# Kernel tuning notes

Measured on AMD Instinct MI355X. Metric: run time of the kernel, lower is better.

Reference implementation:

```python
import jax, jax.numpy as jnp
import numpy as np

B, N, C, K, S = 2, 20000, 64, 16, 4  # batch, points, channels, neighbors, share_planes
CS = C // S
EPS = 1e-5


def _gather(x, idx):
    # x: [B, C, N], idx: [B, N, K] -> [B, C, N, K]
    return jax.vmap(lambda xb, ib: xb[:, ib])(x, idx)


def _bn(x, g, b, m, v):
    # inference-mode BatchNorm2d over channel axis 1; x: [B, C, N, K]
    scale = (g / jnp.sqrt(v + EPS))[None, :, None, None]
    return (x - m[None, :, None, None]) * scale + b[None, :, None, None]


def setup_inputs() -> dict:
    key = jax.random.key(0)
    ks = jax.random.split(key, 32)
    d = {}
    d["coord"] = jax.random.normal(ks[0], (B, N, 3), jnp.float32)
    d["q"] = jax.random.normal(ks[1], (B, C, N), jnp.float32)
    d["k"] = jax.random.normal(ks[2], (B, C, N), jnp.float32)
    d["neighbor_indices"] = jax.random.randint(ks[3], (B, N, K), 0, N, jnp.int32)
    sc = 1.0 / np.sqrt(C)
    d["wq"] = jax.random.normal(ks[4], (C, C), jnp.float32) * sc
    d["bq"] = jnp.zeros((C,), jnp.float32)
    d["wk"] = jax.random.normal(ks[5], (C, C), jnp.float32) * sc
    d["bk"] = jnp.zeros((C,), jnp.float32)
    d["wv"] = jax.random.normal(ks[6], (C, C), jnp.float32) * sc
    d["bv"] = jnp.zeros((C,), jnp.float32)
    # linear_p: Conv2d(3,3,1) -> BN(3) -> ReLU -> Conv2d(3,C,1)
    d["p1_w"] = jax.random.normal(ks[7], (3, 3), jnp.float32) * 0.5
    d["p1_b"] = jnp.zeros((3,), jnp.float32)
    d["p_bn_g"] = jnp.ones((3,), jnp.float32)
    d["p_bn_b"] = jnp.zeros((3,), jnp.float32)
    d["p_bn_m"] = jax.random.normal(ks[8], (3,), jnp.float32) * 0.1
    d["p_bn_v"] = jax.random.uniform(ks[9], (3,), jnp.float32) + 0.5
    d["p2_w"] = jax.random.normal(ks[10], (C, 3), jnp.float32) * 0.5
    d["p2_b"] = jnp.zeros((C,), jnp.float32)
    # linear_w: BN(C) -> ReLU -> Conv2d(C, C//S, 1) -> BN(C//S) -> ReLU -> Conv2d(C//S, C//S, 1)
    d["w_bn1_g"] = jnp.ones((C,), jnp.float32)
    d["w_bn1_b"] = jnp.zeros((C,), jnp.float32)
    d["w_bn1_m"] = jax.random.normal(ks[11], (C,), jnp.float32) * 0.1
    d["w_bn1_v"] = jax.random.uniform(ks[12], (C,), jnp.float32) + 0.5
    d["w1_w"] = jax.random.normal(ks[13], (CS, C), jnp.float32) * sc
    d["w1_b"] = jnp.zeros((CS,), jnp.float32)
    d["w_bn2_g"] = jnp.ones((CS,), jnp.float32)
    d["w_bn2_b"] = jnp.zeros((CS,), jnp.float32)
    d["w_bn2_m"] = jax.random.normal(ks[14], (CS,), jnp.float32) * 0.1
    d["w_bn2_v"] = jax.random.uniform(ks[15], (CS,), jnp.float32) + 0.5
    d["w2_w"] = jax.random.normal(ks[16], (CS, CS), jnp.float32) / np.sqrt(CS)
    d["w2_b"] = jnp.zeros((CS,), jnp.float32)
    return d


def reference(coord, q, k, neighbor_indices, wq, bq, wk, bk, wv, bv,
              p1_w, p1_b, p_bn_g, p_bn_b, p_bn_m, p_bn_v, p2_w, p2_b,
              w_bn1_g, w_bn1_b, w_bn1_m, w_bn1_v, w1_w, w1_b,
              w_bn2_g, w_bn2_b, w_bn2_m, w_bn2_v, w2_w, w2_b):
    # 1x1 Conv1d projections: [B, C, N]
    x_q = jnp.einsum('oc,bcn->bon', wq, q) + bq[None, :, None]
    x_k = jnp.einsum('oc,bcn->bon', wk, k) + bk[None, :, None]
    x_v = jnp.einsum('oc,bcn->bon', wv, q) + bv[None, :, None]
    # KNN gathers -> [B, *, N, K]
    p_r = _gather(jnp.swapaxes(coord, 1, 2), neighbor_indices)  # [B, 3, N, K]
    x_k = _gather(x_k, neighbor_indices)                        # [B, C, N, K]
    x_v = _gather(x_v, neighbor_indices)                        # [B, C, N, K]
    # positional MLP
    p_r = jnp.einsum('oc,bcnk->bonk', p1_w, p_r) + p1_b[None, :, None, None]
    p_r = jax.nn.relu(_bn(p_r, p_bn_g, p_bn_b, p_bn_m, p_bn_v))
    p_r = jnp.einsum('oc,bcnk->bonk', p2_w, p_r) + p2_b[None, :, None, None]  # [B, C, N, K]
    # attention weights MLP
    w = x_k - x_q[:, :, :, None] + p_r                          # [B, C, N, K]
    w = jax.nn.relu(_bn(w, w_bn1_g, w_bn1_b, w_bn1_m, w_bn1_v))
    w = jnp.einsum('oc,bcnk->bonk', w1_w, w) + w1_b[None, :, None, None]      # [B, C/S, N, K]
    w = jax.nn.relu(_bn(w, w_bn2_g, w_bn2_b, w_bn2_m, w_bn2_v))
    w = jnp.einsum('oc,bcnk->bonk', w2_w, w) + w2_b[None, :, None, None]
    w = jax.nn.softmax(w, axis=-1)                              # softmax over K
    # grouped weighted sum
    v = jnp.transpose(x_v + p_r, (0, 2, 3, 1)).reshape(B, N, K, S, CS)  # [B, N, K, S, C/S]
    wp = jnp.transpose(w, (0, 2, 3, 1))                                  # [B, N, K, C/S]
    x = jnp.einsum('bnksg,bnkg->bnsg', v, wp).reshape(B, N, C)
    return jnp.transpose(x, (0, 2, 1))  # [B, C, N]
```

## Files before the change

kernel.cpp:

```cpp
#include <hip/hip_runtime.h>
#include <math.h>

#define B_ 2
#define N_ 20000
#define C_ 64
#define K_ 16
#define CS_ 16
#define EPS_ 1e-5f

typedef float f32x4_t  __attribute__((ext_vector_type(4)));
typedef short bf16x8_t __attribute__((ext_vector_type(8)));
typedef short bf16x4_t __attribute__((ext_vector_type(4)));

__device__ __forceinline__ unsigned int bfbits(float f)
{
    unsigned int b = __builtin_bit_cast(unsigned int, f);
    return (b + 0x7FFFu + ((b >> 16) & 1u)) >> 16;
}
__device__ __forceinline__ float bf_lo(unsigned int w)
{
    return __builtin_bit_cast(float, w << 16);
}
__device__ __forceinline__ float bf_hi(unsigned int w)
{
    return __builtin_bit_cast(float, w & 0xFFFF0000u);
}
__device__ __forceinline__ void wave_fence()
{
    __builtin_amdgcn_wave_barrier();
}
__device__ __forceinline__ unsigned int pk2(const float* p)
{
    return bfbits(p[0]) | (bfbits(p[1]) << 16);
}

__global__ __launch_bounds__(256) void setup_kernel(
    const float* __restrict__ wq, const float* __restrict__ wk,
    const float* __restrict__ wv,
    const float* __restrict__ w1_w, const float* __restrict__ w1_b,
    const float* __restrict__ w2_w, const float* __restrict__ w2_b,
    const float* __restrict__ w_bn2_g, const float* __restrict__ w_bn2_b,
    const float* __restrict__ w_bn2_m, const float* __restrict__ w_bn2_v,
    uint4* __restrict__ wtab, uint4* __restrict__ a1tab,
    uint2* __restrict__ a2tab, float* __restrict__ cz)
{
    const int t = threadIdx.x;
    for (int e = t; e < 1536; e += 256) {
        int m = e >> 9, rem = e & 511;
        int og = rem >> 7, half = (rem >> 6) & 1, l = rem & 63;
        const float* W = (m == 0) ? wq : ((m == 1) ? wk : wv);
        const float* base = W + (size_t)(og * 16 + (l & 15)) * C_ + half * 32 + (l >> 4) * 8;
        uint4 o;
        o.x = pk2(base + 0); o.y = pk2(base + 2);
        o.z = pk2(base + 4); o.w = pk2(base + 6);
        wtab[e] = o;
    }
    if (t < 128) {
        int half = t >> 6, l = t & 63;
        const float* base = w1_w + (size_t)(l & 15) * C_ + half * 32 + (l >> 4) * 8;
        uint4 o;
        o.x = pk2(base + 0); o.y = pk2(base + 2);
        o.z = pk2(base + 4); o.w = pk2(base + 6);
        a1tab[t] = o;
    }
    if (t < 64) {
        const float* base = w2_w + (t & 15) * 16 + (t >> 4) * 4;
        uint2 o;
        o.x = pk2(base + 0); o.y = pk2(base + 2);
        a2tab[t] = o;
    }
    if (t < 16) {
        float s = w_bn2_g[t] * rsqrtf(w_bn2_v[t] + EPS_);
        cz[t]      = s;
        cz[16 + t] = (w1_b[t] - w_bn2_m[t]) * s + w_bn2_b[t];
        cz[32 + t] = w2_b[t];
    }
}

__global__ __launch_bounds__(256) void proj_kernel(
    const float* __restrict__ q, const float* __restrict__ kin,
    const float* __restrict__ coord,
    const float* __restrict__ bq, const float* __restrict__ bk,
    const float* __restrict__ bv,
    const float* __restrict__ p1_w, const float* __restrict__ p1_b,
    const float* __restrict__ p_bn_g, const float* __restrict__ p_bn_b,
    const float* __restrict__ p_bn_m, const float* __restrict__ p_bn_v,
    const float* __restrict__ p2_w, const float* __restrict__ p2_b,
    const float* __restrict__ w_bn1_g, const float* __restrict__ w_bn1_b,
    const float* __restrict__ w_bn1_m, const float* __restrict__ w_bn1_v,
    const uint4* __restrict__ wtab,
    float* __restrict__ xq2, unsigned int* __restrict__ kv_t)
{
    constexpr int PS = 26;
    __shared__ unsigned int qp[32 * PS];
    __shared__ unsigned int kp[32 * PS];

    const int t   = threadIdx.x;
    const int og  = __builtin_amdgcn_readfirstlane(t >> 6);
    const int l   = t & 63;
    const int col = l & 15;
    const int qd  = l >> 4;
    const int pt0 = blockIdx.x * 16;
    const int pt  = pt0 + col;
    const int b   = pt0 / N_;
    const int n   = pt - b * N_;
    const size_t cb = (size_t)b * C_ * N_ + n;

#pragma unroll
    for (int r = 0; r < 2; r++) {
        int cp = (og << 3) + (qd << 1) + r;
        int ci = cp * 2;
        float q0 = q[cb + (size_t)ci * N_];
        float q1 = q[cb + (size_t)(ci + 1) * N_];
        float k0 = kin[cb + (size_t)ci * N_];
        float k1 = kin[cb + (size_t)(ci + 1) * N_];
        qp[cp * PS + col] = bfbits(q0) | (bfbits(q1) << 16);
        kp[cp * PS + col] = bfbits(k0) | (bfbits(k1) << 16);
    }

    union bf8u { bf16x8_t v; uint4 u4; };
    bf8u awq[2], awk[2], awv[2];
#pragma unroll
    for (int half = 0; half < 2; half++) {
        awq[half].u4 = wtab[0 * 512 + og * 128 + half * 64 + l];
        awk[half].u4 = wtab[1 * 512 + og * 128 + half * 64 + l];
        awv[half].u4 = wtab[2 * 512 + og * 128 + half * 64 + l];
    }

    __syncthreads();

    union bf8b { bf16x8_t v; unsigned int u[4]; };
    bf8b bq_[2], bk_[2];
#pragma unroll
    for (int half = 0; half < 2; half++) {
#pragma unroll
        for (int i2 = 0; i2 < 4; i2++) {
            int cp = half * 16 + qd * 4 + i2;
            bq_[half].u[i2] = qp[cp * PS + col];
            bk_[half].u[i2] = kp[cp * PS + col];
        }
    }

    f32x4_t uq = {0.f, 0.f, 0.f, 0.f};
    f32x4_t uv = {0.f, 0.f, 0.f, 0.f};
    f32x4_t uk = {0.f, 0.f, 0.f, 0.f};
    uq = __builtin_amdgcn_mfma_f32_16x16x32_bf16(awq[0].v, bq_[0].v, uq, 0, 0, 0);
    uq = __builtin_amdgcn_mfma_f32_16x16x32_bf16(awq[1].v, bq_[1].v, uq, 0, 0, 0);
    uv = __builtin_amdgcn_mfma_f32_16x16x32_bf16(awv[0].v, bq_[0].v, uv, 0, 0, 0);
    uv = __builtin_amdgcn_mfma_f32_16x16x32_bf16(awv[1].v, bq_[1].v, uv, 0, 0, 0);
    uk = __builtin_amdgcn_mfma_f32_16x16x32_bf16(awk[0].v, bk_[0].v, uk, 0, 0, 0);
    uk = __builtin_amdgcn_mfma_f32_16x16x32_bf16(awk[1].v, bk_[1].v, uk, 0, 0, 0);

    float pbs[3], pbb[3];
#pragma unroll
    for (int j = 0; j < 3; j++) {
        float s = p_bn_g[j] * rsqrtf(p_bn_v[j] + EPS_);
        pbs[j] = s;
        pbb[j] = (p1_b[j] - p_bn_m[j]) * s + p_bn_b[j];
    }
    float cx = coord[pt * 3 + 0], cy = coord[pt * 3 + 1], cz = coord[pt * 3 + 2];
    float h0 = fmaxf(0.f, (p1_w[0]*cx + p1_w[1]*cy + p1_w[2]*cz) * pbs[0] + pbb[0]);
    float h1 = fmaxf(0.f, (p1_w[3]*cx + p1_w[4]*cy + p1_w[5]*cz) * pbs[1] + pbb[1]);
    float h2 = fmaxf(0.f, (p1_w[6]*cx + p1_w[7]*cy + p1_w[8]*cz) * pbs[2] + pbb[2]);

    const int ch0 = og * 16 + qd * 4;
    float pos[4];
#pragma unroll
    for (int rr = 0; rr < 4; rr++) {
        int ch = ch0 + rr;
        pos[rr] = fmaf(p2_w[ch*3+0], h0, fmaf(p2_w[ch*3+1], h1,
                  fmaf(p2_w[ch*3+2], h2, p2_b[ch])));
    }

    const float4 bqv = *reinterpret_cast<const float4*>(bq + ch0);
    const float4 bkv = *reinterpret_cast<const float4*>(bk + ch0);
    const float4 bvv = *reinterpret_cast<const float4*>(bv + ch0);
    const float4 g1  = *reinterpret_cast<const float4*>(w_bn1_g + ch0);
    const float4 b1  = *reinterpret_cast<const float4*>(w_bn1_b + ch0);
    const float4 m1  = *reinterpret_cast<const float4*>(w_bn1_m + ch0);
    const float4 v1  = *reinterpret_cast<const float4*>(w_bn1_v + ch0);

    float4 xqo;
    uint4 kvo;
#pragma unroll
    for (int rr = 0; rr < 4; rr++) {
        float s   = (&g1.x)[rr] * rsqrtf((&v1.x)[rr] + EPS_);
        float b1f = (&b1.x)[rr] - (&m1.x)[rr] * s;
        float xqv = uq[rr] + (&bqv.x)[rr];
        (&xqo.x)[rr] = s * xqv - b1f;
        float kk = s * (uk[rr] + (&bkv.x)[rr] + pos[rr]);
        float vv = uv[rr] + (&bvv.x)[rr] + pos[rr];
        (&kvo.x)[rr] = bfbits(kk) | (bfbits(vv) << 16);
    }
    *reinterpret_cast<float4*>(xq2 + (size_t)pt * C_ + ch0) = xqo;
    *reinterpret_cast<uint4*>(kv_t + (size_t)pt * C_ + ch0) = kvo;
}

#define WROW 72
#define WPN  (K_ * WROW)
#define SS4  20
#define SPN  (K_ * SS4)

__global__ __launch_bounds__(1024, 8) void attn_kernel(
    const int* __restrict__ nbr,
    const float* __restrict__ xq2, const unsigned int* __restrict__ kv_t,
    const uint4* __restrict__ a1tab, const uint2* __restrict__ a2tab,
    const float* __restrict__ cz,
    float* __restrict__ out)
{
    __shared__ unsigned short wlds_all[16 * WPN];
    __shared__ float          sfb_all[16 * SPN];
    __shared__ float          otile[64 * 17];

    const int w  = __builtin_amdgcn_readfirstlane(threadIdx.x >> 6);
    const int l  = threadIdx.x & 63;
    const int al = l & 15;
    const int qd = l >> 4;
    const int cpair = l & 31;
    const int kh    = l >> 5;
    const int c0    = cpair * 2;

    const int pt0 = blockIdx.x * 16;
    const int b   = pt0 / N_;
    const int bB  = b * N_;
    const int bn  = pt0 + w;

    unsigned short* wlds = wlds_all + w * WPN;
    float*          sfb  = sfb_all + w * SPN;

    union bf8u { bf16x8_t v; uint4 u4; };
    union bf4u { bf16x4_t v; uint2 u2; };
    bf8u a1q0, a1q1; bf4u a2q;
    a1q0.u4 = a1tab[l];
    a1q1.u4 = a1tab[64 + l];
    a2q.u2  = a2tab[l];
    const float4 zsc4 = *reinterpret_cast<const float4*>(cz + qd * 4);
    const float4 zbi4 = *reinterpret_cast<const float4*>(cz + 16 + qd * 4);
    const float4 tbi4 = *reinterpret_cast<const float4*>(cz + 32 + qd * 4);
    const float2 xqp  = *reinterpret_cast<const float2*>(xq2 + (size_t)bn * C_ + c0);

    const int* nb = nbr + (size_t)bn * K_;
    uint2 kvw[8];
#pragma unroll
    for (int j = 0; j < 8; j++) {
        int ia = nb[j];
        int ib = nb[8 + j];
        int idx = (kh != 0) ? ib : ia;
        kvw[j] = *reinterpret_cast<const uint2*>(kv_t + ((size_t)(bB + idx) * C_ + c0));
    }
#pragma unroll
    for (int j = 0; j < 8; j++) {
        float w0 = fmaxf(0.f, bf_lo(kvw[j].x) - xqp.x);
        float w1 = fmaxf(0.f, bf_lo(kvw[j].y) - xqp.y);
        unsigned int pkw = bfbits(w0) | (bfbits(w1) << 16);
        *reinterpret_cast<unsigned int*>(wlds + (kh * 8 + j) * WROW + c0) = pkw;
    }
    wave_fence();

    const bf16x8_t b0 = *reinterpret_cast<const bf16x8_t*>(wlds + al * WROW + qd * 8);
    const bf16x8_t b1 = *reinterpret_cast<const bf16x8_t*>(wlds + al * WROW + 32 + qd * 8);
    f32x4_t u = {0.f, 0.f, 0.f, 0.f};
    u = __builtin_amdgcn_mfma_f32_16x16x32_bf16(a1q0.v, b0, u, 0, 0, 0);
    u = __builtin_amdgcn_mfma_f32_16x16x32_bf16(a1q1.v, b1, u, 0, 0, 0);

    union { bf16x4_t v; unsigned int u2[2]; } zb;
    {
        float z0 = fmaxf(0.f, u[0] * zsc4.x + zbi4.x);
        float z1 = fmaxf(0.f, u[1] * zsc4.y + zbi4.y);
        float z2 = fmaxf(0.f, u[2] * zsc4.z + zbi4.z);
        float z3 = fmaxf(0.f, u[3] * zsc4.w + zbi4.w);
        zb.u2[0] = bfbits(z0) | (bfbits(z1) << 16);
        zb.u2[1] = bfbits(z2) | (bfbits(z3) << 16);
    }

    f32x4_t t4 = {0.f, 0.f, 0.f, 0.f};
    t4 = __builtin_amdgcn_mfma_f32_16x16x16bf16_1k(a2q.v, zb.v, t4, 0, 0, 0);

    float4 sv;
#pragma unroll
    for (int rr = 0; rr < 4; rr++) {
        float e = __expf(t4[rr] + (&tbi4.x)[rr]);
        float s = e;
        s += __shfl_xor(s, 1);
        s += __shfl_xor(s, 2);
        s += __shfl_xor(s, 4);
        s += __shfl_xor(s, 8);
        (&sv.x)[rr] = e * __builtin_amdgcn_rcpf(s);
    }
    *reinterpret_cast<float4*>(sfb + al * SS4 + qd * 4) = sv;
    wave_fence();

    const int g0 = c0 & 15;
    float acc0 = 0.f, acc1 = 0.f;
#pragma unroll
    for (int j = 0; j < 8; j++) {
        float2 sp = *reinterpret_cast<const float2*>(sfb + (kh * 8 + j) * SS4 + g0);
        acc0 = fmaf(bf_hi(kvw[j].x), sp.x, acc0);
        acc1 = fmaf(bf_hi(kvw[j].y), sp.y, acc1);
    }
    acc0 += __shfl_xor(acc0, 32);
    acc1 += __shfl_xor(acc1, 32);
    if (kh == 0) {
        otile[c0 * 17 + w]       = acc0;
        otile[(c0 + 1) * 17 + w] = acc1;
    }
    __syncthreads();

    {
        int c  = threadIdx.x >> 4;
        int nn = threadIdx.x & 15;
        out[(size_t)b * C_ * N_ + (size_t)c * N_ + (pt0 - bB) + nn] = otile[c * 17 + nn];
    }
}

extern "C" void kernel_launch(void* const* d_in, const int* in_sizes, int n_in,
                              void* d_out, int out_size, void* d_ws, size_t ws_size,
                              hipStream_t stream)
{
    const float* coord = (const float*)d_in[0];
    const float* q     = (const float*)d_in[1];
    const float* k     = (const float*)d_in[2];
    const int*   nbr   = (const int*)d_in[3];
    const float* wq = (const float*)d_in[4];
    const float* bq = (const float*)d_in[5];
    const float* wk = (const float*)d_in[6];
    const float* bk = (const float*)d_in[7];
    const float* wv = (const float*)d_in[8];
    const float* bv = (const float*)d_in[9];
    const float* p1_w = (const float*)d_in[10];
    const float* p1_b = (const float*)d_in[11];
    const float* p_bn_g = (const float*)d_in[12];
    const float* p_bn_b = (const float*)d_in[13];
    const float* p_bn_m = (const float*)d_in[14];
    const float* p_bn_v = (const float*)d_in[15];
    const float* p2_w = (const float*)d_in[16];
    const float* p2_b = (const float*)d_in[17];
    const float* w_bn1_g = (const float*)d_in[18];
    const float* w_bn1_b = (const float*)d_in[19];
    const float* w_bn1_m = (const float*)d_in[20];
    const float* w_bn1_v = (const float*)d_in[21];
    const float* w1_w = (const float*)d_in[22];
    const float* w1_b = (const float*)d_in[23];
    const float* w_bn2_g = (const float*)d_in[24];
    const float* w_bn2_b = (const float*)d_in[25];
    const float* w_bn2_m = (const float*)d_in[26];
    const float* w_bn2_v = (const float*)d_in[27];
    const float* w2_w = (const float*)d_in[28];
    const float* w2_b = (const float*)d_in[29];

    const size_t PTS = (size_t)B_ * N_;
    float* ws = (float*)d_ws;
    float* xq2 = ws;
    unsigned int* kv_t = (unsigned int*)(ws + PTS * C_);
    uint4* wtab  = (uint4*)(ws + 2 * PTS * C_);
    uint4* a1tab = wtab + 1536;
    uint2* a2tab = (uint2*)(a1tab + 128);
    float* cz    = (float*)(a2tab + 64);

    setup_kernel<<<1, 256, 0, stream>>>(
        wq, wk, wv, w1_w, w1_b, w2_w, w2_b,
        w_bn2_g, w_bn2_b, w_bn2_m, w_bn2_v,
        wtab, a1tab, a2tab, cz);

    proj_kernel<<<(B_ * N_) / 16, 256, 0, stream>>>(
        q, k, coord, bq, bk, bv,
        p1_w, p1_b, p_bn_g, p_bn_b, p_bn_m, p_bn_v, p2_w, p2_b,
        w_bn1_g, w_bn1_b, w_bn1_m, w_bn1_v,
        wtab, xq2, kv_t);

    attn_kernel<<<(B_ * N_) / 16, 1024, 0, stream>>>(
        nbr, xq2, kv_t, a1tab, a2tab, cz,
        (float*)d_out);
}
```

Baseline: 49.39 us.

## Store xq in bf16, use hardware bf16 packing, hoist gathers, parallelize setup

The xq intermediate is stored as packed bf16 instead of fp32, which halves its write and read traffic between the projection and attention kernels. The manual round-to-nearest-even bf16 packing is replaced with the HIP __float22bfloat162_rn intrinsic, which may lower to a packed hardware conversion. The neighbor index loads and kv gathers are moved to the start of the attention kernel to increase memory-level parallelism. The setup kernel is spread over six blocks instead of one loop. Rounding xq to bf16 adds precision loss in the attention-weight input.

```diff
diff --git a/kernel.cpp b/kernel.cpp
--- a/kernel.cpp
+++ b/kernel.cpp
@@ -1,4 +1,5 @@
 #include <hip/hip_runtime.h>
+#include <hip/hip_bf16.h>
 #include <math.h>
 
 #define B_ 2
@@ -12,10 +13,11 @@
 typedef short bf16x8_t __attribute__((ext_vector_type(8)));
 typedef short bf16x4_t __attribute__((ext_vector_type(4)));
 
-__device__ __forceinline__ unsigned int bfbits(float f)
-{
-    unsigned int b = __builtin_bit_cast(unsigned int, f);
-    return (b + 0x7FFFu + ((b >> 16) & 1u)) >> 16;
+__device__ __forceinline__ unsigned int packbf2(float a, float b)
+{
+    union { __hip_bfloat162 h; unsigned int u; } cv;
+    cv.h = __float22bfloat162_rn(float2{a, b});
+    return cv.u;
 }
 __device__ __forceinline__ float bf_lo(unsigned int w)
 {
@@ -28,10 +30,6 @@
 __device__ __forceinline__ void wave_fence()
 {
     __builtin_amdgcn_wave_barrier();
-}
-__device__ __forceinline__ unsigned int pk2(const float* p)
-{
-    return bfbits(p[0]) | (bfbits(p[1]) << 16);
 }
 
 __global__ __launch_bounds__(256) void setup_kernel(
@@ -44,32 +42,34 @@
     uint4* __restrict__ wtab, uint4* __restrict__ a1tab,
     uint2* __restrict__ a2tab, float* __restrict__ cz)
 {
-    const int t = threadIdx.x;
-    for (int e = t; e < 1536; e += 256) {
+    const int t   = threadIdx.x;
+    const int blk = blockIdx.x;
+    {
+        int e = blk * 256 + t;
         int m = e >> 9, rem = e & 511;
         int og = rem >> 7, half = (rem >> 6) & 1, l = rem & 63;
         const float* W = (m == 0) ? wq : ((m == 1) ? wk : wv);
         const float* base = W + (size_t)(og * 16 + (l & 15)) * C_ + half * 32 + (l >> 4) * 8;
         uint4 o;
-        o.x = pk2(base + 0); o.y = pk2(base + 2);
-        o.z = pk2(base + 4); o.w = pk2(base + 6);
+        o.x = packbf2(base[0], base[1]); o.y = packbf2(base[2], base[3]);
+        o.z = packbf2(base[4], base[5]); o.w = packbf2(base[6], base[7]);
         wtab[e] = o;
     }
-    if (t < 128) {
+    if (blk == 0 && t < 128) {
         int half = t >> 6, l = t & 63;
         const float* base = w1_w + (size_t)(l & 15) * C_ + half * 32 + (l >> 4) * 8;
         uint4 o;
-        o.x = pk2(base + 0); o.y = pk2(base + 2);
-        o.z = pk2(base + 4); o.w = pk2(base + 6);
+        o.x = packbf2(base[0], base[1]); o.y = packbf2(base[2], base[3]);
+        o.z = packbf2(base[4], base[5]); o.w = packbf2(base[6], base[7]);
         a1tab[t] = o;
     }
-    if (t < 64) {
+    if (blk == 1 && t < 64) {
         const float* base = w2_w + (t & 15) * 16 + (t >> 4) * 4;
         uint2 o;
-        o.x = pk2(base + 0); o.y = pk2(base + 2);
+        o.x = packbf2(base[0], base[1]); o.y = packbf2(base[2], base[3]);
         a2tab[t] = o;
     }
-    if (t < 16) {
+    if (blk == 2 && t < 16) {
         float s = w_bn2_g[t] * rsqrtf(w_bn2_v[t] + EPS_);
         cz[t]      = s;
         cz[16 + t] = (w1_b[t] - w_bn2_m[t]) * s + w_bn2_b[t];
@@ -89,7 +89,7 @@
     const float* __restrict__ w_bn1_g, const float* __restrict__ w_bn1_b,
     const float* __restrict__ w_bn1_m, const float* __restrict__ w_bn1_v,
     const uint4* __restrict__ wtab,
-    float* __restrict__ xq2, unsigned int* __restrict__ kv_t)
+    unsigned int* __restrict__ xq2, unsigned int* __restrict__ kv_t)
 {
     constexpr int PS = 26;
     __shared__ unsigned int qp[32 * PS];
@@ -114,8 +114,8 @@
         float q1 = q[cb + (size_t)(ci + 1) * N_];
         float k0 = kin[cb + (size_t)ci * N_];
         float k1 = kin[cb + (size_t)(ci + 1) * N_];
-        qp[cp * PS + col] = bfbits(q0) | (bfbits(q1) << 16);
-        kp[cp * PS + col] = bfbits(k0) | (bfbits(k1) << 16);
+        qp[cp * PS + col] = packbf2(q0, q1);
+        kp[cp * PS + col] = packbf2(k0, k1);
     }
 
     union bf8u { bf16x8_t v; uint4 u4; };
@@ -180,19 +180,21 @@
     const float4 m1  = *reinterpret_cast<const float4*>(w_bn1_m + ch0);
     const float4 v1  = *reinterpret_cast<const float4*>(w_bn1_v + ch0);
 
-    float4 xqo;
+    float xv2[4];
     uint4 kvo;
 #pragma unroll
     for (int rr = 0; rr < 4; rr++) {
         float s   = (&g1.x)[rr] * rsqrtf((&v1.x)[rr] + EPS_);
         float b1f = (&b1.x)[rr] - (&m1.x)[rr] * s;
-        float xqv = uq[rr] + (&bqv.x)[rr];
-        (&xqo.x)[rr] = s * xqv - b1f;
-        float kk = s * (uk[rr] + (&bkv.x)[rr] + pos[rr]);
-        float vv = uv[rr] + (&bvv.x)[rr] + pos[rr];
-        (&kvo.x)[rr] = bfbits(kk) | (bfbits(vv) << 16);
-    }
-    *reinterpret_cast<float4*>(xq2 + (size_t)pt * C_ + ch0) = xqo;
+        xv2[rr]   = s * (uq[rr] + (&bqv.x)[rr]) - b1f;
+        float kk  = s * (uk[rr] + (&bkv.x)[rr] + pos[rr]);
+        float vv  = uv[rr] + (&bvv.x)[rr] + pos[rr];
+        (&kvo.x)[rr] = packbf2(kk, vv);
+    }
+    uint2 xqo;
+    xqo.x = packbf2(xv2[0], xv2[1]);
+    xqo.y = packbf2(xv2[2], xv2[3]);
+    *reinterpret_cast<uint2*>(xq2 + (size_t)pt * 32 + (ch0 >> 1)) = xqo;
     *reinterpret_cast<uint4*>(kv_t + (size_t)pt * C_ + ch0) = kvo;
 }
 
@@ -203,7 +205,7 @@
 
 __global__ __launch_bounds__(1024, 8) void attn_kernel(
     const int* __restrict__ nbr,
-    const float* __restrict__ xq2, const unsigned int* __restrict__ kv_t,
+    const unsigned int* __restrict__ xq2, const unsigned int* __restrict__ kv_t,
     const uint4* __restrict__ a1tab, const uint2* __restrict__ a2tab,
     const float* __restrict__ cz,
     float* __restrict__ out)
@@ -227,6 +229,19 @@
 
     unsigned short* wlds = wlds_all + w * WPN;
     float*          sfb  = sfb_all + w * SPN;
+
+    const int* nb = nbr + (size_t)bn * K_;
+    uint2 kvw[8];
+#pragma unroll
+    for (int j = 0; j < 8; j++) {
+        int ia = nb[j];
+        int ib = nb[8 + j];
+        int idx = (kh != 0) ? ib : ia;
+        kvw[j] = *reinterpret_cast<const uint2*>(kv_t + ((size_t)(bB + idx) * C_ + c0));
+    }
+    const unsigned int xqu = xq2[(size_t)bn * 32 + cpair];
+    const float xq0 = bf_lo(xqu);
+    const float xq1 = bf_hi(xqu);
 
     union bf8u { bf16x8_t v; uint4 u4; };
     union bf4u { bf16x4_t v; uint2 u2; };
@@ -237,23 +252,12 @@
     const float4 zsc4 = *reinterpret_cast<const float4*>(cz + qd * 4);
     const float4 zbi4 = *reinterpret_cast<const float4*>(cz + 16 + qd * 4);
     const float4 tbi4 = *reinterpret_cast<const float4*>(cz + 32 + qd * 4);
-    const float2 xqp  = *reinterpret_cast<const float2*>(xq2 + (size_t)bn * C_ + c0);
-
-    const int* nb = nbr + (size_t)bn * K_;
-    uint2 kvw[8];
+
 #pragma unroll
     for (int j = 0; j < 8; j++) {
-        int ia = nb[j];
-        int ib = nb[8 + j];
-        int idx = (kh != 0) ? ib : ia;
-        kvw[j] = *reinterpret_cast<const uint2*>(kv_t + ((size_t)(bB + idx) * C_ + c0));
-    }
-#pragma unroll
-    for (int j = 0; j < 8; j++) {
-        float w0 = fmaxf(0.f, bf_lo(kvw[j].x) - xqp.x);
-        float w1 = fmaxf(0.f, bf_lo(kvw[j].y) - xqp.y);
-        unsigned int pkw = bfbits(w0) | (bfbits(w1) << 16);
-        *reinterpret_cast<unsigned int*>(wlds + (kh * 8 + j) * WROW + c0) = pkw;
+        float w0 = fmaxf(0.f, bf_lo(kvw[j].x) - xq0);
+        float w1 = fmaxf(0.f, bf_lo(kvw[j].y) - xq1);
+        *reinterpret_cast<unsigned int*>(wlds + (kh * 8 + j) * WROW + c0) = packbf2(w0, w1);
     }
     wave_fence();
 
@@ -269,8 +273,8 @@
         float z1 = fmaxf(0.f, u[1] * zsc4.y + zbi4.y);
         float z2 = fmaxf(0.f, u[2] * zsc4.z + zbi4.z);
         float z3 = fmaxf(0.f, u[3] * zsc4.w + zbi4.w);
-        zb.u2[0] = bfbits(z0) | (bfbits(z1) << 16);
-        zb.u2[1] = bfbits(z2) | (bfbits(z3) << 16);
+        zb.u2[0] = packbf2(z0, z1);
+        zb.u2[1] = packbf2(z2, z3);
     }
 
     f32x4_t t4 = {0.f, 0.f, 0.f, 0.f};
@@ -349,15 +353,15 @@
     const float* w2_b = (const float*)d_in[29];
 
     const size_t PTS = (size_t)B_ * N_;
-    float* ws = (float*)d_ws;
-    float* xq2 = ws;
-    unsigned int* kv_t = (unsigned int*)(ws + PTS * C_);
-    uint4* wtab  = (uint4*)(ws + 2 * PTS * C_);
+    char* wsb = (char*)d_ws;
+    unsigned int* kv_t = (unsigned int*)wsb;
+    unsigned int* xq2  = (unsigned int*)(wsb + PTS * C_ * 4);
+    uint4* wtab  = (uint4*)(wsb + PTS * C_ * 4 + PTS * C_ * 2);
     uint4* a1tab = wtab + 1536;
     uint2* a2tab = (uint2*)(a1tab + 128);
     float* cz    = (float*)(a2tab + 64);
 
-    setup_kernel<<<1, 256, 0, stream>>>(
+    setup_kernel<<<6, 256, 0, stream>>>(
         wq, wk, wv, w1_w, w1_b, w2_w, w2_b,
         w_bn2_g, w_bn2_b, w_bn2_m, w_bn2_v,
         wtab, a1tab, a2tab, cz);
```

After: 48.07 us. 2.7% less time.
